# Performance work log

Measured on AMD Instinct MI355X. Metric: run time of the kernel, lower is better.

## Reference

```python
import jax, jax.numpy as jnp
import numpy as np

BN_EPS = 1e-5


def l2norm(x, axis=-1):
    # matches lavse l2norm: x / sqrt(sum(x^2)) along axis
    return x / jnp.sqrt(jnp.sum(x * x, axis=axis, keepdims=True))


def mlp(x, W1, b1, W2, b2):
    # nn.Sequential(Linear, ReLU, Linear)
    return jax.nn.relu(x @ W1 + b1) @ W2 + b2


def setup_inputs() -> dict:
    key = jax.random.key(0)
    ks = jax.random.split(key, 12)
    B, R, T, D, H = 128, 36, 64, 1024, 128  # batch, regions, max words, latent, D//k
    s = 0.02
    return {
        "img_embed": jax.random.normal(ks[0], (B, R, D), jnp.float32),
        "cap_embed": jax.random.normal(ks[1], (B, T, D), jnp.float32),
        "lens": jax.random.randint(ks[2], (B,), 1, T + 1),
        "Wg1": jax.random.normal(ks[3], (D, H), jnp.float32) * s,
        "bg1": jnp.zeros((H,), jnp.float32),
        "Wg2": jax.random.normal(ks[4], (H, D), jnp.float32) * s,
        "bg2": jnp.zeros((D,), jnp.float32),
        "Wb1": jax.random.normal(ks[5], (D, H), jnp.float32) * s,
        "bb1": jnp.zeros((H,), jnp.float32),
        "Wb2": jax.random.normal(ks[6], (H, D), jnp.float32) * s,
        "bb2": jnp.zeros((D,), jnp.float32),
    }


def reference(img_embed, cap_embed, lens, Wg1, bg1, Wg2, bg2, Wb1, bb1, Wb2, bb2):
    # img_embed: (Bi, R, D); cap_embed: (Bc, T, D); lens: (Bc,) int
    Bc, T, D = cap_embed.shape
    dt = cap_embed.dtype

    # masked mean-pool of caption words (cap_tensor[:, :n_words].mean(-1))
    mask = (jnp.arange(T)[None, :] < lens[:, None]).astype(dt)          # (Bc, T)
    cap_repr = jnp.einsum('btd,bt->bd', cap_embed, mask) / lens[:, None].astype(dt)  # (Bc, D)

    # conditional BN gamma/beta from caption representation
    gamma = mlp(cap_repr, Wg1, bg1, Wg2, bg2)                           # (Bc, D)
    beta = mlp(cap_repr, Wb1, bb1, Wb2, bb2)                            # (Bc, D)

    # BatchNorm1d(affine=False, training): per-channel stats over batch & regions
    mean = jnp.mean(img_embed, axis=(0, 1))                             # (D,)
    var = jnp.mean((img_embed - mean) ** 2, axis=(0, 1))                # biased var, (D,)
    norm_img = (img_embed - mean) / jnp.sqrt(var + BN_EPS)              # (Bi, R, D)
    norm_mean = jnp.mean(norm_img, axis=1)                              # (Bi, D), mean over regions

    # conditioned image vectors per caption: affine then l2norm
    img_vec = norm_mean[None, :, :] * (1.0 + gamma[:, None, :]) + beta[:, None, :]  # (Bc, Bi, D)
    img_vec = l2norm(img_vec, axis=-1)
    cap_vec = l2norm(cap_repr, axis=-1)                                 # (Bc, D)

    # cosine_sim(img_vector, cap_vector): dot of unit vectors; sims[:, i] = sim
    sims = jnp.einsum('cbd,cd->bc', img_vec, cap_vec)                   # (Bi, Bc)
    return sims
```

## Files before the change

### kernel.cpp

```cpp
#include <hip/hip_runtime.h>

#define DD 1024
#define TT 64
#define RR 36
#define NBC 128
#define NBI 128
#define HH 128

#define OFF_CAPR 0
#define OFF_CAPU (128 * 1024)
#define OFF_S    (2 * 128 * 1024)
#define OFF_P    (3 * 128 * 1024)
#define OFF_G1   (4 * 128 * 1024)
#define OFF_BETA (5 * 128 * 1024)
#define OFF_A    (6 * 128 * 1024)
#define OFF_BV   (6 * 128 * 1024 + 1024)
#define OFF_H    (6 * 128 * 1024 + 2048)

__device__ __forceinline__ float4 f4add(float4 a, float4 b) {
    return make_float4(a.x + b.x, a.y + b.y, a.z + b.z, a.w + b.w);
}

__global__ __launch_bounds__(256) void k_pool(const float* __restrict__ img,
                                              const float* __restrict__ cap,
                                              const int* __restrict__ lens,
                                              float* __restrict__ ws) {
    const int tid = threadIdx.x;
    const int blk = blockIdx.x;
    __shared__ float red[4];

    if (blk < NBC) {
        const int b = blk;
        const int len = lens[b];
        const float4* cp = (const float4*)(cap + (size_t)b * TT * DD);
        float4 a0 = make_float4(0.f, 0.f, 0.f, 0.f);
        float4 a1 = a0, a2 = a0, a3 = a0, a4 = a0, a5 = a0, a6 = a0, a7 = a0;
        int w = 0;
        for (; w + 8 <= len; w += 8) {
            const float4* p = cp + (size_t)w * (DD / 4) + tid;
            float4 x0 = p[0 * (DD / 4)];
            float4 x1 = p[1 * (DD / 4)];
            float4 x2 = p[2 * (DD / 4)];
            float4 x3 = p[3 * (DD / 4)];
            float4 x4 = p[4 * (DD / 4)];
            float4 x5 = p[5 * (DD / 4)];
            float4 x6 = p[6 * (DD / 4)];
            float4 x7 = p[7 * (DD / 4)];
            a0 = f4add(a0, x0); a1 = f4add(a1, x1);
            a2 = f4add(a2, x2); a3 = f4add(a3, x3);
            a4 = f4add(a4, x4); a5 = f4add(a5, x5);
            a6 = f4add(a6, x6); a7 = f4add(a7, x7);
        }
        for (; w < len; ++w) a0 = f4add(a0, cp[(size_t)w * (DD / 4) + tid]);
        float4 acc = f4add(f4add(f4add(a0, a1), f4add(a2, a3)),
                           f4add(f4add(a4, a5), f4add(a6, a7)));
        const float inv = 1.0f / (float)len;
        acc.x *= inv; acc.y *= inv; acc.z *= inv; acc.w *= inv;
        ((float4*)(ws + OFF_CAPR + (size_t)b * DD))[tid] = acc;

        float ss = acc.x * acc.x + acc.y * acc.y + acc.z * acc.z + acc.w * acc.w;
        #pragma unroll
        for (int o = 32; o; o >>= 1) ss += __shfl_xor(ss, o);
        if ((tid & 63) == 0) red[tid >> 6] = ss;
        __syncthreads();
        const float tot = red[0] + red[1] + red[2] + red[3];
        const float rn = rsqrtf(tot);
        float4 u = make_float4(acc.x * rn, acc.y * rn, acc.z * rn, acc.w * rn);
        ((float4*)(ws + OFF_CAPU + (size_t)b * DD))[tid] = u;
    } else {
        const int b = blk - NBC;
        const float4* ip = (const float4*)(img + (size_t)b * RR * DD);
        float4 s0 = make_float4(0.f, 0.f, 0.f, 0.f), s1 = s0;
        float4 q0 = s0, q1 = s0;
        #pragma unroll 3
        for (int r = 0; r < RR; r += 2) {
            float4 x = ip[r * (DD / 4) + tid];
            float4 y = ip[(r + 1) * (DD / 4) + tid];
            s0 = f4add(s0, x);
            q0.x = fmaf(x.x, x.x, q0.x); q0.y = fmaf(x.y, x.y, q0.y);
            q0.z = fmaf(x.z, x.z, q0.z); q0.w = fmaf(x.w, x.w, q0.w);
            s1 = f4add(s1, y);
            q1.x = fmaf(y.x, y.x, q1.x); q1.y = fmaf(y.y, y.y, q1.y);
            q1.z = fmaf(y.z, y.z, q1.z); q1.w = fmaf(y.w, y.w, q1.w);
        }
        ((float4*)(ws + OFF_S + (size_t)b * DD))[tid] = f4add(s0, s1);
        ((float4*)(ws + OFF_P + (size_t)b * DD))[tid] = f4add(q0, q1);
    }
}

__global__ __launch_bounds__(256) void k_mlp1(
        const float* __restrict__ Wg1, const float* __restrict__ bg1,
        const float* __restrict__ Wb1, const float* __restrict__ bb1,
        float* __restrict__ ws) {
    const int blk = blockIdx.x;
    const int tid = threadIdx.x;

    if (blk >= 256) {
        const int dl = tid & 63;
        const int d = (blk - 256) * 64 + dl;
        const int bq = tid >> 6;
        float s = 0.f, q = 0.f;
        #pragma unroll 4
        for (int i = 0; i < 32; ++i) {
            const int b = bq * 32 + i;
            s += ws[OFF_S + (size_t)b * DD + d];
            q += ws[OFF_P + (size_t)b * DD + d];
        }
        __shared__ float rs[4][64], rq[4][64];
        rs[bq][dl] = s; rq[bq][dl] = q;
        __syncthreads();
        if (bq == 0) {
            s = rs[0][dl] + rs[1][dl] + rs[2][dl] + rs[3][dl];
            q = rq[0][dl] + rq[1][dl] + rq[2][dl] + rq[3][dl];
            const float invN = 1.0f / (float)(NBI * RR);
            const float mean = s * invN;
            const float var = q * invN - mean * mean;
            const float rstd = rsqrtf(var + 1e-5f);
            ws[OFF_A + d] = rstd * (1.0f / (float)RR);
            ws[OFF_BV + d] = mean * rstd;
        }
        return;
    }

    const int cg = blk >> 4;
    const int net = (blk >> 3) & 1;
    const int jq = blk & 7;
    const int c0 = cg * 8, j0 = jq * 16;
    const int j16 = tid & 15;
    const int ks = tid >> 4;
    const float* __restrict__ W1 = net ? Wb1 : Wg1;
    const float* __restrict__ b1 = net ? bb1 : bg1;

    __shared__ float capL[8][DD];
    {
        const float4* src = (const float4*)(ws + OFF_CAPR);
        #pragma unroll
        for (int i = 0; i < 8; ++i) {
            const int idx = i * 256 + tid;
            const int c = idx >> 8, f4 = idx & 255;
            ((float4*)&capL[c][0])[f4] = src[(size_t)(c0 + c) * 256 + f4];
        }
    }
    __syncthreads();

    float a[8] = {0.f, 0.f, 0.f, 0.f, 0.f, 0.f, 0.f, 0.f};
    #pragma unroll
    for (int i = 0; i < 16; ++i) {
        const int d = i * 64 + ks * 4;
        const float w0 = W1[(size_t)(d + 0) * HH + j0 + j16];
        const float w1 = W1[(size_t)(d + 1) * HH + j0 + j16];
        const float w2 = W1[(size_t)(d + 2) * HH + j0 + j16];
        const float w3 = W1[(size_t)(d + 3) * HH + j0 + j16];
        #pragma unroll
        for (int c = 0; c < 8; ++c) {
            const float4 cv = *(const float4*)&capL[c][d];
            a[c] = fmaf(w0, cv.x, a[c]);
            a[c] = fmaf(w1, cv.y, a[c]);
            a[c] = fmaf(w2, cv.z, a[c]);
            a[c] = fmaf(w3, cv.w, a[c]);
        }
    }
    #pragma unroll
    for (int c = 0; c < 8; ++c) {
        a[c] += __shfl_xor(a[c], 16);
        a[c] += __shfl_xor(a[c], 32);
    }
    __shared__ float part[4][16][8];
    const int wv = tid >> 6;
    if ((tid & 48) == 0) {
        #pragma unroll
        for (int c = 0; c < 8; ++c) part[wv][j16][c] = a[c];
    }
    __syncthreads();
    if (tid < 128) {
        const int cc = tid >> 4, jj = tid & 15;
        float h = part[0][jj][cc] + part[1][jj][cc] + part[2][jj][cc] +
                  part[3][jj][cc] + b1[j0 + jj];
        h = fmaxf(h, 0.0f);
        ws[OFF_H + ((size_t)(c0 + cc) * 2 + net) * HH + j0 + jj] = h;
    }
}

__global__ __launch_bounds__(256) void k_mlp2(
        const float* __restrict__ Wg2, const float* __restrict__ bg2,
        const float* __restrict__ Wb2, const float* __restrict__ bb2,
        float* __restrict__ ws) {
    const int blk = blockIdx.x;
    const int cg = blk >> 4;
    const int net = (blk >> 3) & 1;
    const int dq = blk & 7;
    const int c0 = cg * 8, ch0 = dq * 128;
    const int tid = threadIdx.x;
    const float* __restrict__ W2 = net ? Wb2 : Wg2;
    const float* __restrict__ b2 = net ? bb2 : bg2;

    __shared__ float hL[8][HH];
    {
        const int c = tid >> 5, j4 = tid & 31;
        ((float4*)&hL[c][0])[j4] =
            ((const float4*)(ws + OFF_H + ((size_t)(c0 + c) * 2 + net) * HH))[j4];
    }
    __syncthreads();

    const int c = tid >> 5, q = tid & 31;
    const int ch = ch0 + q * 4;
    float4 acA = make_float4(0.f, 0.f, 0.f, 0.f);
    float4 acB = acA, acC = acA, acD = acA;
    #pragma unroll 2
    for (int j = 0; j < HH; j += 4) {
        const float4 w0 = *(const float4*)&W2[(size_t)(j + 0) * DD + ch];
        const float4 w1 = *(const float4*)&W2[(size_t)(j + 1) * DD + ch];
        const float4 w2 = *(const float4*)&W2[(size_t)(j + 2) * DD + ch];
        const float4 w3 = *(const float4*)&W2[(size_t)(j + 3) * DD + ch];
        const float h0 = hL[c][j + 0], h1 = hL[c][j + 1];
        const float h2 = hL[c][j + 2], h3 = hL[c][j + 3];
        acA.x = fmaf(h0, w0.x, acA.x); acA.y = fmaf(h0, w0.y, acA.y);
        acA.z = fmaf(h0, w0.z, acA.z); acA.w = fmaf(h0, w0.w, acA.w);
        acB.x = fmaf(h1, w1.x, acB.x); acB.y = fmaf(h1, w1.y, acB.y);
        acB.z = fmaf(h1, w1.z, acB.z); acB.w = fmaf(h1, w1.w, acB.w);
        acC.x = fmaf(h2, w2.x, acC.x); acC.y = fmaf(h2, w2.y, acC.y);
        acC.z = fmaf(h2, w2.z, acC.z); acC.w = fmaf(h2, w2.w, acC.w);
        acD.x = fmaf(h3, w3.x, acD.x); acD.y = fmaf(h3, w3.y, acD.y);
        acD.z = fmaf(h3, w3.z, acD.z); acD.w = fmaf(h3, w3.w, acD.w);
    }
    float4 acc = f4add(f4add(acA, acB), f4add(acC, acD));
    const float4 bv = *(const float4*)&b2[ch];
    if (net == 0) {
        float4 g = make_float4(1.f + acc.x + bv.x, 1.f + acc.y + bv.y,
                               1.f + acc.z + bv.z, 1.f + acc.w + bv.w);
        *(float4*)(ws + OFF_G1 + (size_t)(c0 + c) * DD + ch) = g;
    } else {
        float4 be = make_float4(acc.x + bv.x, acc.y + bv.y,
                                acc.z + bv.z, acc.w + bv.w);
        *(float4*)(ws + OFF_BETA + (size_t)(c0 + c) * DD + ch) = be;
    }
}

__global__ __launch_bounds__(256) void k_sims(const float* __restrict__ ws,
                                              float* __restrict__ out) {
    const int c = blockIdx.x;
    const int bg = blockIdx.y;
    const int lane = threadIdx.x & 63;
    const int w = threadIdx.x >> 6;

    const float4* Ap = (const float4*)(ws + OFF_A);
    const float4* Bp = (const float4*)(ws + OFF_BV);
    const float4* Gp = (const float4*)(ws + OFF_G1 + (size_t)c * DD);
    const float4* Ep = (const float4*)(ws + OFF_BETA + (size_t)c * DD);
    const float4* Up = (const float4*)(ws + OFF_CAPU + (size_t)c * DD);

    float4 AG[4], BB[4], CU[4];
    #pragma unroll
    for (int i = 0; i < 4; ++i) {
        const int idx = i * 64 + lane;
        const float4 a = Ap[idx];
        const float4 bv = Bp[idx];
        const float4 g = Gp[idx];
        const float4 be = Ep[idx];
        AG[i] = make_float4(a.x * g.x, a.y * g.y, a.z * g.z, a.w * g.w);
        BB[i] = make_float4(be.x - bv.x * g.x, be.y - bv.y * g.y,
                            be.z - bv.z * g.z, be.w - bv.w * g.w);
        CU[i] = Up[idx];
    }

    const float4* Sp = (const float4*)(ws + OFF_S);
    #pragma unroll
    for (int ib = 0; ib < 8; ++ib) {
        const int b = bg * 32 + w * 8 + ib;
        float dot = 0.f, ss = 0.f;
        #pragma unroll
        for (int i = 0; i < 4; ++i) {
            const float4 s4 = Sp[(size_t)b * (DD / 4) + i * 64 + lane];
            const float vx = fmaf(s4.x, AG[i].x, BB[i].x);
            const float vy = fmaf(s4.y, AG[i].y, BB[i].y);
            const float vz = fmaf(s4.z, AG[i].z, BB[i].z);
            const float vw = fmaf(s4.w, AG[i].w, BB[i].w);
            ss = fmaf(vx, vx, fmaf(vy, vy, fmaf(vz, vz, fmaf(vw, vw, ss))));
            dot = fmaf(vx, CU[i].x, fmaf(vy, CU[i].y,
                  fmaf(vz, CU[i].z, fmaf(vw, CU[i].w, dot))));
        }
        #pragma unroll
        for (int o = 32; o; o >>= 1) {
            dot += __shfl_xor(dot, o);
            ss += __shfl_xor(ss, o);
        }
        if (lane == 0) out[b * NBC + c] = dot * rsqrtf(ss);
    }
}

extern "C" void kernel_launch(void* const* d_in, const int* in_sizes, int n_in,
                              void* d_out, int out_size, void* d_ws, size_t ws_size,
                              hipStream_t stream) {
    const float* img = (const float*)d_in[0];
    const float* cap = (const float*)d_in[1];
    const int* lens  = (const int*)d_in[2];
    const float* Wg1 = (const float*)d_in[3];
    const float* bg1 = (const float*)d_in[4];
    const float* Wg2 = (const float*)d_in[5];
    const float* bg2 = (const float*)d_in[6];
    const float* Wb1 = (const float*)d_in[7];
    const float* bb1 = (const float*)d_in[8];
    const float* Wb2 = (const float*)d_in[9];
    const float* bb2 = (const float*)d_in[10];
    float* ws = (float*)d_ws;
    float* out = (float*)d_out;

    hipLaunchKernelGGL(k_pool, dim3(256), dim3(256), 0, stream, img, cap, lens, ws);
    hipLaunchKernelGGL(k_mlp1, dim3(272), dim3(256), 0, stream,
                       Wg1, bg1, Wb1, bb1, ws);
    hipLaunchKernelGGL(k_mlp2, dim3(256), dim3(256), 0, stream,
                       Wg2, bg2, Wb2, bb2, ws);
    hipLaunchKernelGGL(k_sims, dim3(128, 4), dim3(256), 0, stream, ws, out);
}
```

Baseline: 128.5 us.

## Fuse four kernels into one cooperative kernel with grid-wide syncs

Merges pooling, MLP layer 1, MLP layer 2 plus BN stats, and the similarity stage into one cooperative kernel of 256 blocks separated by grid.sync(). The aim is to remove three kernel launch gaps and their tail effects. MLP2 is retiled to 16 captions per block over 128 blocks, and the final stage uses 2 blocks per caption instead of 4. If the cooperative launch fails it falls back to the old four-kernel path. Grid barriers cost extra, and the heavy shared-memory footprint must still allow all 256 blocks to be co-resident.

```diff
diff --git a/kernel.cpp b/kernel.cpp
--- a/kernel.cpp
+++ b/kernel.cpp
@@ -1,4 +1,7 @@
 #include <hip/hip_runtime.h>
+#include <hip/hip_cooperative_groups.h>
+
+namespace cg = cooperative_groups;
 
 #define DD 1024
 #define TT 64
@@ -7,27 +10,38 @@
 #define NBI 128
 #define HH 128
 
+#define SEG (128 * 1024)
 #define OFF_CAPR 0
-#define OFF_CAPU (128 * 1024)
-#define OFF_S    (2 * 128 * 1024)
-#define OFF_P    (3 * 128 * 1024)
-#define OFF_G1   (4 * 128 * 1024)
-#define OFF_BETA (5 * 128 * 1024)
-#define OFF_A    (6 * 128 * 1024)
-#define OFF_BV   (6 * 128 * 1024 + 1024)
-#define OFF_H    (6 * 128 * 1024 + 2048)
+#define OFF_CAPU (1 * SEG)
+#define OFF_S    (2 * SEG)
+#define OFF_P    (3 * SEG)
+#define OFF_G1   (4 * SEG)
+#define OFF_BETA (5 * SEG)
+#define OFF_A    (6 * SEG)
+#define OFF_BV   (6 * SEG + 1024)
+#define OFF_H    (6 * SEG + 2048)
 
 __device__ __forceinline__ float4 f4add(float4 a, float4 b) {
     return make_float4(a.x + b.x, a.y + b.y, a.z + b.z, a.w + b.w);
 }
 
-__global__ __launch_bounds__(256) void k_pool(const float* __restrict__ img,
-                                              const float* __restrict__ cap,
-                                              const int* __restrict__ lens,
-                                              float* __restrict__ ws) {
+__global__ __launch_bounds__(256) void k_fused(
+        const float* __restrict__ img, const float* __restrict__ cap,
+        const int* __restrict__ lens,
+        const float* __restrict__ Wg1, const float* __restrict__ bg1,
+        const float* __restrict__ Wg2, const float* __restrict__ bg2,
+        const float* __restrict__ Wb1, const float* __restrict__ bb1,
+        const float* __restrict__ Wb2, const float* __restrict__ bb2,
+        float* __restrict__ ws, float* __restrict__ out) {
+    cg::grid_group grid = cg::this_grid();
+    const int blk = blockIdx.x;
     const int tid = threadIdx.x;
-    const int blk = blockIdx.x;
-    __shared__ float red[4];
+
+    __shared__ float capL[8][DD];
+    __shared__ float part[4][16][8];
+    __shared__ float hL[16][HH];
+    __shared__ float rs[4][64], rq[4][64];
+    __shared__ float red4[4];
 
     if (blk < NBC) {
         const int b = blk;
@@ -61,6 +75,267 @@
         float ss = acc.x * acc.x + acc.y * acc.y + acc.z * acc.z + acc.w * acc.w;
         #pragma unroll
         for (int o = 32; o; o >>= 1) ss += __shfl_xor(ss, o);
+        if ((tid & 63) == 0) red4[tid >> 6] = ss;
+        __syncthreads();
+        const float tot = red4[0] + red4[1] + red4[2] + red4[3];
+        const float rn = rsqrtf(tot);
+        float4 u = make_float4(acc.x * rn, acc.y * rn, acc.z * rn, acc.w * rn);
+        ((float4*)(ws + OFF_CAPU + (size_t)b * DD))[tid] = u;
+    } else {
+        const int b = blk - NBC;
+        const float4* ip = (const float4*)(img + (size_t)b * RR * DD);
+        float4 s0 = make_float4(0.f, 0.f, 0.f, 0.f), s1 = s0;
+        float4 q0 = s0, q1 = s0;
+        #pragma unroll 3
+        for (int r = 0; r < RR; r += 2) {
+            float4 x = ip[r * (DD / 4) + tid];
+            float4 y = ip[(r + 1) * (DD / 4) + tid];
+            s0 = f4add(s0, x);
+            q0.x = fmaf(x.x, x.x, q0.x); q0.y = fmaf(x.y, x.y, q0.y);
+            q0.z = fmaf(x.z, x.z, q0.z); q0.w = fmaf(x.w, x.w, q0.w);
+            s1 = f4add(s1, y);
+            q1.x = fmaf(y.x, y.x, q1.x); q1.y = fmaf(y.y, y.y, q1.y);
+            q1.z = fmaf(y.z, y.z, q1.z); q1.w = fmaf(y.w, y.w, q1.w);
+        }
+        ((float4*)(ws + OFF_S + (size_t)b * DD))[tid] = f4add(s0, s1);
+        ((float4*)(ws + OFF_P + (size_t)b * DD))[tid] = f4add(q0, q1);
+    }
+
+    grid.sync();
+
+    {
+        const int cg_ = blk >> 4;
+        const int net = (blk >> 3) & 1;
+        const int jq = blk & 7;
+        const int c0 = cg_ * 8, j0 = jq * 16;
+        const int j16 = tid & 15;
+        const int ks = tid >> 4;
+        const float* __restrict__ W1 = net ? Wb1 : Wg1;
+        const float* __restrict__ b1 = net ? bb1 : bg1;
+
+        {
+            const float4* src = (const float4*)(ws + OFF_CAPR);
+            #pragma unroll
+            for (int i = 0; i < 8; ++i) {
+                ((float4*)&capL[i][0])[tid] = src[(size_t)(c0 + i) * 256 + tid];
+            }
+        }
+        __syncthreads();
+
+        float a[8] = {0.f, 0.f, 0.f, 0.f, 0.f, 0.f, 0.f, 0.f};
+        #pragma unroll
+        for (int i = 0; i < 16; ++i) {
+            const int d = i * 64 + ks * 4;
+            const float w0 = W1[(size_t)(d + 0) * HH + j0 + j16];
+            const float w1 = W1[(size_t)(d + 1) * HH + j0 + j16];
+            const float w2 = W1[(size_t)(d + 2) * HH + j0 + j16];
+            const float w3 = W1[(size_t)(d + 3) * HH + j0 + j16];
+            #pragma unroll
+            for (int c = 0; c < 8; ++c) {
+                const float4 cv = *(const float4*)&capL[c][d];
+                a[c] = fmaf(w0, cv.x, a[c]);
+                a[c] = fmaf(w1, cv.y, a[c]);
+                a[c] = fmaf(w2, cv.z, a[c]);
+                a[c] = fmaf(w3, cv.w, a[c]);
+            }
+        }
+        #pragma unroll
+        for (int c = 0; c < 8; ++c) {
+            a[c] += __shfl_xor(a[c], 16);
+            a[c] += __shfl_xor(a[c], 32);
+        }
+        const int wv = tid >> 6;
+        if ((tid & 48) == 0) {
+            #pragma unroll
+            for (int c = 0; c < 8; ++c) part[wv][j16][c] = a[c];
+        }
+        __syncthreads();
+        if (tid < 128) {
+            const int cc = tid >> 4, jj = tid & 15;
+            float h = part[0][jj][cc] + part[1][jj][cc] + part[2][jj][cc] +
+                      part[3][jj][cc] + b1[j0 + jj];
+            h = fmaxf(h, 0.0f);
+            ws[OFF_H + ((size_t)(c0 + cc) * 2 + net) * HH + j0 + jj] = h;
+        }
+    }
+
+    grid.sync();
+
+    if (blk < 128) {
+        const int cg_ = blk >> 4;
+        const int net = (blk >> 3) & 1;
+        const int dq = blk & 7;
+        const int c0 = cg_ * 16, ch0 = dq * 128;
+        const float* __restrict__ W2 = net ? Wb2 : Wg2;
+        const float* __restrict__ b2 = net ? bb2 : bg2;
+
+        #pragma unroll
+        for (int i = 0; i < 2; ++i) {
+            const int idx = i * 256 + tid;
+            const int c = idx >> 5, j4 = idx & 31;
+            ((float4*)&hL[c][0])[j4] =
+                ((const float4*)(ws + OFF_H + ((size_t)(c0 + c) * 2 + net) * HH))[j4];
+        }
+        __syncthreads();
+
+        const int c = tid >> 4, q = tid & 15;
+        const int ch = ch0 + q * 8;
+        float4 a0 = make_float4(0.f, 0.f, 0.f, 0.f);
+        float4 a1 = a0, a2 = a0, a3 = a0;
+        #pragma unroll 4
+        for (int j = 0; j < HH; j += 2) {
+            const float4 w0 = *(const float4*)&W2[(size_t)j * DD + ch];
+            const float4 w1 = *(const float4*)&W2[(size_t)j * DD + ch + 4];
+            const float4 w2_ = *(const float4*)&W2[(size_t)(j + 1) * DD + ch];
+            const float4 w3 = *(const float4*)&W2[(size_t)(j + 1) * DD + ch + 4];
+            const float h0 = hL[c][j], h1 = hL[c][j + 1];
+            a0.x = fmaf(h0, w0.x, a0.x); a0.y = fmaf(h0, w0.y, a0.y);
+            a0.z = fmaf(h0, w0.z, a0.z); a0.w = fmaf(h0, w0.w, a0.w);
+            a1.x = fmaf(h0, w1.x, a1.x); a1.y = fmaf(h0, w1.y, a1.y);
+            a1.z = fmaf(h0, w1.z, a1.z); a1.w = fmaf(h0, w1.w, a1.w);
+            a2.x = fmaf(h1, w2_.x, a2.x); a2.y = fmaf(h1, w2_.y, a2.y);
+            a2.z = fmaf(h1, w2_.z, a2.z); a2.w = fmaf(h1, w2_.w, a2.w);
+            a3.x = fmaf(h1, w3.x, a3.x); a3.y = fmaf(h1, w3.y, a3.y);
+            a3.z = fmaf(h1, w3.z, a3.z); a3.w = fmaf(h1, w3.w, a3.w);
+        }
+        float4 r0 = f4add(a0, a2);
+        float4 r1 = f4add(a1, a3);
+        const float4 b2a = *(const float4*)&b2[ch];
+        const float4 b2b = *(const float4*)&b2[ch + 4];
+        if (net == 0) {
+            float4 g0 = make_float4(1.f + r0.x + b2a.x, 1.f + r0.y + b2a.y,
+                                    1.f + r0.z + b2a.z, 1.f + r0.w + b2a.w);
+            float4 g1v = make_float4(1.f + r1.x + b2b.x, 1.f + r1.y + b2b.y,
+                                     1.f + r1.z + b2b.z, 1.f + r1.w + b2b.w);
+            *(float4*)(ws + OFF_G1 + (size_t)(c0 + c) * DD + ch) = g0;
+            *(float4*)(ws + OFF_G1 + (size_t)(c0 + c) * DD + ch + 4) = g1v;
+        } else {
+            float4 e0 = make_float4(r0.x + b2a.x, r0.y + b2a.y,
+                                    r0.z + b2a.z, r0.w + b2a.w);
+            float4 e1 = make_float4(r1.x + b2b.x, r1.y + b2b.y,
+                                    r1.z + b2b.z, r1.w + b2b.w);
+            *(float4*)(ws + OFF_BETA + (size_t)(c0 + c) * DD + ch) = e0;
+            *(float4*)(ws + OFF_BETA + (size_t)(c0 + c) * DD + ch + 4) = e1;
+        }
+    } else if (blk < 144) {
+        const int dl = tid & 63;
+        const int d = (blk - 128) * 64 + dl;
+        const int bq = tid >> 6;
+        float s = 0.f, q = 0.f;
+        #pragma unroll 4
+        for (int i = 0; i < 32; ++i) {
+            const int b = bq * 32 + i;
+            s += ws[OFF_S + (size_t)b * DD + d];
+            q += ws[OFF_P + (size_t)b * DD + d];
+        }
+        rs[bq][dl] = s; rq[bq][dl] = q;
+        __syncthreads();
+        if (bq == 0) {
+            s = rs[0][dl] + rs[1][dl] + rs[2][dl] + rs[3][dl];
+            q = rq[0][dl] + rq[1][dl] + rq[2][dl] + rq[3][dl];
+            const float invN = 1.0f / (float)(NBI * RR);
+            const float mean = s * invN;
+            const float var = q * invN - mean * mean;
+            const float rstd = rsqrtf(var + 1e-5f);
+            ws[OFF_A + d] = rstd * (1.0f / (float)RR);
+            ws[OFF_BV + d] = mean * rstd;
+        }
+    }
+
+    grid.sync();
+
+    {
+        const int c = blk >> 1;
+        const int bg = blk & 1;
+        const int lane = tid & 63;
+        const int w = tid >> 6;
+
+        const float4* Ap = (const float4*)(ws + OFF_A);
+        const float4* Bp = (const float4*)(ws + OFF_BV);
+        const float4* Gp = (const float4*)(ws + OFF_G1 + (size_t)c * DD);
+        const float4* Ep = (const float4*)(ws + OFF_BETA + (size_t)c * DD);
+        const float4* Up = (const float4*)(ws + OFF_CAPU + (size_t)c * DD);
+
+        float4 AG[4], BB[4], CU[4];
+        #pragma unroll
+        for (int i = 0; i < 4; ++i) {
+            const int idx = i * 64 + lane;
+            const float4 a = Ap[idx];
+            const float4 bv = Bp[idx];
+            const float4 g = Gp[idx];
+            const float4 be = Ep[idx];
+            AG[i] = make_float4(a.x * g.x, a.y * g.y, a.z * g.z, a.w * g.w);
+            BB[i] = make_float4(be.x - bv.x * g.x, be.y - bv.y * g.y,
+                                be.z - bv.z * g.z, be.w - bv.w * g.w);
+            CU[i] = Up[idx];
+        }
+
+        const float4* Sp = (const float4*)(ws + OFF_S);
+        #pragma unroll
+        for (int ib = 0; ib < 16; ++ib) {
+            const int b = bg * 64 + w * 16 + ib;
+            float dot = 0.f, ss = 0.f;
+            #pragma unroll
+            for (int i = 0; i < 4; ++i) {
+                const float4 s4 = Sp[(size_t)b * (DD / 4) + i * 64 + lane];
+                const float vx = fmaf(s4.x, AG[i].x, BB[i].x);
+                const float vy = fmaf(s4.y, AG[i].y, BB[i].y);
+                const float vz = fmaf(s4.z, AG[i].z, BB[i].z);
+                const float vw = fmaf(s4.w, AG[i].w, BB[i].w);
+                ss = fmaf(vx, vx, fmaf(vy, vy, fmaf(vz, vz, fmaf(vw, vw, ss))));
+                dot = fmaf(vx, CU[i].x, fmaf(vy, CU[i].y,
+                      fmaf(vz, CU[i].z, fmaf(vw, CU[i].w, dot))));
+            }
+            #pragma unroll
+            for (int o = 32; o; o >>= 1) {
+                dot += __shfl_xor(dot, o);
+                ss += __shfl_xor(ss, o);
+            }
+            if (lane == 0) out[b * NBC + c] = dot * rsqrtf(ss);
+        }
+    }
+}
+
+__global__ __launch_bounds__(256) void k_pool(const float* __restrict__ img,
+                                              const float* __restrict__ cap,
+                                              const int* __restrict__ lens,
+                                              float* __restrict__ ws) {
+    const int tid = threadIdx.x;
+    const int blk = blockIdx.x;
+    __shared__ float red[4];
+
+    if (blk < NBC) {
+        const int b = blk;
+        const int len = lens[b];
+        const float4* cp = (const float4*)(cap + (size_t)b * TT * DD);
+        float4 a0 = make_float4(0.f, 0.f, 0.f, 0.f);
+        float4 a1 = a0, a2 = a0, a3 = a0, a4 = a0, a5 = a0, a6 = a0, a7 = a0;
+        int w = 0;
+        for (; w + 8 <= len; w += 8) {
+            const float4* p = cp + (size_t)w * (DD / 4) + tid;
+            float4 x0 = p[0 * (DD / 4)];
+            float4 x1 = p[1 * (DD / 4)];
+            float4 x2 = p[2 * (DD / 4)];
+            float4 x3 = p[3 * (DD / 4)];
+            float4 x4 = p[4 * (DD / 4)];
+            float4 x5 = p[5 * (DD / 4)];
+            float4 x6 = p[6 * (DD / 4)];
+            float4 x7 = p[7 * (DD / 4)];
+            a0 = f4add(a0, x0); a1 = f4add(a1, x1);
+            a2 = f4add(a2, x2); a3 = f4add(a3, x3);
+            a4 = f4add(a4, x4); a5 = f4add(a5, x5);
+            a6 = f4add(a6, x6); a7 = f4add(a7, x7);
+        }
+        for (; w < len; ++w) a0 = f4add(a0, cp[(size_t)w * (DD / 4) + tid]);
+        float4 acc = f4add(f4add(f4add(a0, a1), f4add(a2, a3)),
+                           f4add(f4add(a4, a5), f4add(a6, a7)));
+        const float inv = 1.0f / (float)len;
+        acc.x *= inv; acc.y *= inv; acc.z *= inv; acc.w *= inv;
+        ((float4*)(ws + OFF_CAPR + (size_t)b * DD))[tid] = acc;
+
+        float ss = acc.x * acc.x + acc.y * acc.y + acc.z * acc.z + acc.w * acc.w;
+        #pragma unroll
+        for (int o = 32; o; o >>= 1) ss += __shfl_xor(ss, o);
         if ((tid & 63) == 0) red[tid >> 6] = ss;
         __syncthreads();
         const float tot = red[0] + red[1] + red[2] + red[3];
@@ -122,10 +397,10 @@
         return;
     }
 
-    const int cg = blk >> 4;
+    const int cg_ = blk >> 4;
     const int net = (blk >> 3) & 1;
     const int jq = blk & 7;
-    const int c0 = cg * 8, j0 = jq * 16;
+    const int c0 = cg_ * 8, j0 = jq * 16;
     const int j16 = tid & 15;
     const int ks = tid >> 4;
     const float* __restrict__ W1 = net ? Wb1 : Wg1;
@@ -136,9 +411,7 @@
         const float4* src = (const float4*)(ws + OFF_CAPR);
         #pragma unroll
         for (int i = 0; i < 8; ++i) {
-            const int idx = i * 256 + tid;
-            const int c = idx >> 8, f4 = idx & 255;
-            ((float4*)&capL[c][0])[f4] = src[(size_t)(c0 + c) * 256 + f4];
+            ((float4*)&capL[i][0])[tid] = src[(size_t)(c0 + i) * 256 + tid];
         }
     }
     __syncthreads();
@@ -186,10 +459,10 @@
         const float* __restrict__ Wb2, const float* __restrict__ bb2,
         float* __restrict__ ws) {
     const int blk = blockIdx.x;
-    const int cg = blk >> 4;
+    const int cg_ = blk >> 4;
     const int net = (blk >> 3) & 1;
     const int dq = blk & 7;
-    const int c0 = cg * 8, ch0 = dq * 128;
+    const int c0 = cg_ * 8, ch0 = dq * 128;
     const int tid = threadIdx.x;
     const float* __restrict__ W2 = net ? Wb2 : Wg2;
     const float* __restrict__ b2 = net ? bb2 : bg2;
@@ -305,10 +578,21 @@
     float* ws = (float*)d_ws;
     float* out = (float*)d_out;
 
-    hipLaunchKernelGGL(k_pool, dim3(256), dim3(256), 0, stream, img, cap, lens, ws);
-    hipLaunchKernelGGL(k_mlp1, dim3(272), dim3(256), 0, stream,
-                       Wg1, bg1, Wb1, bb1, ws);
-    hipLaunchKernelGGL(k_mlp2, dim3(256), dim3(256), 0, stream,
-                       Wg2, bg2, Wb2, bb2, ws);
-    hipLaunchKernelGGL(k_sims, dim3(128, 4), dim3(256), 0, stream, ws, out);
-}
+    void* args[] = {(void*)&img, (void*)&cap, (void*)&lens,
+                    (void*)&Wg1, (void*)&bg1, (void*)&Wg2, (void*)&bg2,
+                    (void*)&Wb1, (void*)&bb1, (void*)&Wb2, (void*)&bb2,
+                    (void*)&ws, (void*)&out};
+    hipError_t err = hipLaunchCooperativeKernel((const void*)k_fused,
+                                                dim3(256), dim3(256),
+                                                args, 0, stream);
+    if (err != hipSuccess) {
+        (void)hipGetLastError();
+        hipLaunchKernelGGL(k_pool, dim3(256), dim3(256), 0, stream,
+                           img, cap, lens, ws);
+        hipLaunchKernelGGL(k_mlp1, dim3(272), dim3(256), 0, stream,
+                           Wg1, bg1, Wb1, bb1, ws);
+        hipLaunchKernelGGL(k_mlp2, dim3(256), dim3(256), 0, stream,
+                           Wg2, bg2, Wb2, bb2, ws);
+        hipLaunchKernelGGL(k_sims, dim3(128, 4), dim3(256), 0, stream, ws, out);
+    }
+}
```

After: 241.6 us. +88.1%, slower.

## Split pooling into halves and fuse MLP second layer with similarity kernel

Applied to the files above, without the earlier changes.

The pooling kernel now splits each caption and image batch element across two blocks, writing partial sums that later stages combine. This doubles parallelism in the bandwidth-bound first stage. The second MLP layer is fused into the similarity kernel, so each caption block computes gamma/beta in registers and shared memory, removing one launch and the gamma/beta round trip through global memory. The trade-off is that the final kernel has only 128 blocks, and each block streams both full W2 matrices and all 128 image rows, which may limit parallelism.

```diff
diff --git a/kernel.cpp b/kernel.cpp
--- a/kernel.cpp
+++ b/kernel.cpp
@@ -7,18 +7,24 @@
 #define NBI 128
 #define HH 128
 
-#define OFF_CAPR 0
-#define OFF_CAPU (128 * 1024)
-#define OFF_S    (2 * 128 * 1024)
-#define OFF_P    (3 * 128 * 1024)
-#define OFF_G1   (4 * 128 * 1024)
-#define OFF_BETA (5 * 128 * 1024)
-#define OFF_A    (6 * 128 * 1024)
-#define OFF_BV   (6 * 128 * 1024 + 1024)
-#define OFF_H    (6 * 128 * 1024 + 2048)
+#define SEG (128 * 1024)
+#define OFF_CP0 (0 * SEG)
+#define OFF_CP1 (1 * SEG)
+#define OFF_S0  (2 * SEG)
+#define OFF_S1  (3 * SEG)
+#define OFF_P0  (4 * SEG)
+#define OFF_P1  (5 * SEG)
+#define OFF_S   (6 * SEG)
+#define OFF_A   (7 * SEG)
+#define OFF_BV  (7 * SEG + 1024)
+#define OFF_H   (7 * SEG + 2048)
 
 __device__ __forceinline__ float4 f4add(float4 a, float4 b) {
     return make_float4(a.x + b.x, a.y + b.y, a.z + b.z, a.w + b.w);
+}
+__device__ __forceinline__ float4 f4fma(float s, float4 w, float4 a) {
+    return make_float4(fmaf(s, w.x, a.x), fmaf(s, w.y, a.y),
+                       fmaf(s, w.z, a.z), fmaf(s, w.w, a.w));
 }
 
 __global__ __launch_bounds__(256) void k_pool(const float* __restrict__ img,
@@ -27,16 +33,17 @@
                                               float* __restrict__ ws) {
     const int tid = threadIdx.x;
     const int blk = blockIdx.x;
-    __shared__ float red[4];
-
-    if (blk < NBC) {
-        const int b = blk;
+
+    if (blk < 256) {
+        const int b = blk >> 1, h = blk & 1;
         const int len = lens[b];
+        const int w0 = h * 32;
+        const int w1 = min(len, w0 + 32);
         const float4* cp = (const float4*)(cap + (size_t)b * TT * DD);
         float4 a0 = make_float4(0.f, 0.f, 0.f, 0.f);
         float4 a1 = a0, a2 = a0, a3 = a0, a4 = a0, a5 = a0, a6 = a0, a7 = a0;
-        int w = 0;
-        for (; w + 8 <= len; w += 8) {
+        int w = w0;
+        for (; w + 8 <= w1; w += 8) {
             const float4* p = cp + (size_t)w * (DD / 4) + tid;
             float4 x0 = p[0 * (DD / 4)];
             float4 x1 = p[1 * (DD / 4)];
@@ -51,29 +58,20 @@
             a4 = f4add(a4, x4); a5 = f4add(a5, x5);
             a6 = f4add(a6, x6); a7 = f4add(a7, x7);
         }
-        for (; w < len; ++w) a0 = f4add(a0, cp[(size_t)w * (DD / 4) + tid]);
+        for (; w < w1; ++w) a0 = f4add(a0, cp[(size_t)w * (DD / 4) + tid]);
         float4 acc = f4add(f4add(f4add(a0, a1), f4add(a2, a3)),
                            f4add(f4add(a4, a5), f4add(a6, a7)));
-        const float inv = 1.0f / (float)len;
-        acc.x *= inv; acc.y *= inv; acc.z *= inv; acc.w *= inv;
-        ((float4*)(ws + OFF_CAPR + (size_t)b * DD))[tid] = acc;
-
-        float ss = acc.x * acc.x + acc.y * acc.y + acc.z * acc.z + acc.w * acc.w;
-        #pragma unroll
-        for (int o = 32; o; o >>= 1) ss += __shfl_xor(ss, o);
-        if ((tid & 63) == 0) red[tid >> 6] = ss;
-        __syncthreads();
-        const float tot = red[0] + red[1] + red[2] + red[3];
-        const float rn = rsqrtf(tot);
-        float4 u = make_float4(acc.x * rn, acc.y * rn, acc.z * rn, acc.w * rn);
-        ((float4*)(ws + OFF_CAPU + (size_t)b * DD))[tid] = u;
+        float* dst = ws + (h ? OFF_CP1 : OFF_CP0) + (size_t)b * DD;
+        ((float4*)dst)[tid] = acc;
     } else {
-        const int b = blk - NBC;
-        const float4* ip = (const float4*)(img + (size_t)b * RR * DD);
+        const int t = blk - 256;
+        const int b = t >> 1, h = t & 1;
+        const float4* ip = (const float4*)(img + (size_t)b * RR * DD +
+                                           (size_t)h * 18 * DD);
         float4 s0 = make_float4(0.f, 0.f, 0.f, 0.f), s1 = s0;
         float4 q0 = s0, q1 = s0;
         #pragma unroll 3
-        for (int r = 0; r < RR; r += 2) {
+        for (int r = 0; r < 18; r += 2) {
             float4 x = ip[r * (DD / 4) + tid];
             float4 y = ip[(r + 1) * (DD / 4) + tid];
             s0 = f4add(s0, x);
@@ -83,17 +81,32 @@
             q1.x = fmaf(y.x, y.x, q1.x); q1.y = fmaf(y.y, y.y, q1.y);
             q1.z = fmaf(y.z, y.z, q1.z); q1.w = fmaf(y.w, y.w, q1.w);
         }
-        ((float4*)(ws + OFF_S + (size_t)b * DD))[tid] = f4add(s0, s1);
-        ((float4*)(ws + OFF_P + (size_t)b * DD))[tid] = f4add(q0, q1);
-    }
-}
-
-__global__ __launch_bounds__(256) void k_mlp1(
+        float* sd = ws + (h ? OFF_S1 : OFF_S0) + (size_t)b * DD;
+        float* pd = ws + (h ? OFF_P1 : OFF_P0) + (size_t)b * DD;
+        ((float4*)sd)[tid] = f4add(s0, s1);
+        ((float4*)pd)[tid] = f4add(q0, q1);
+    }
+}
+
+__global__ __launch_bounds__(256) void k_mid(
         const float* __restrict__ Wg1, const float* __restrict__ bg1,
         const float* __restrict__ Wb1, const float* __restrict__ bb1,
+        const int* __restrict__ lens,
         float* __restrict__ ws) {
     const int blk = blockIdx.x;
     const int tid = threadIdx.x;
+
+    __shared__ float capL[8][DD];
+    __shared__ float part[4][16][8];
+    __shared__ float rs[4][64], rq[4][64];
+
+    if (blk >= 272) {
+        const int b = blk - 272;
+        float4 s0 = ((const float4*)(ws + OFF_S0 + (size_t)b * DD))[tid];
+        float4 s1 = ((const float4*)(ws + OFF_S1 + (size_t)b * DD))[tid];
+        ((float4*)(ws + OFF_S + (size_t)b * DD))[tid] = f4add(s0, s1);
+        return;
+    }
 
     if (blk >= 256) {
         const int dl = tid & 63;
@@ -103,10 +116,9 @@
         #pragma unroll 4
         for (int i = 0; i < 32; ++i) {
             const int b = bq * 32 + i;
-            s += ws[OFF_S + (size_t)b * DD + d];
-            q += ws[OFF_P + (size_t)b * DD + d];
-        }
-        __shared__ float rs[4][64], rq[4][64];
+            s += ws[OFF_S0 + (size_t)b * DD + d] + ws[OFF_S1 + (size_t)b * DD + d];
+            q += ws[OFF_P0 + (size_t)b * DD + d] + ws[OFF_P1 + (size_t)b * DD + d];
+        }
         rs[bq][dl] = s; rq[bq][dl] = q;
         __syncthreads();
         if (bq == 0) {
@@ -122,24 +134,24 @@
         return;
     }
 
-    const int cg = blk >> 4;
+    const int cg_ = blk >> 4;
     const int net = (blk >> 3) & 1;
     const int jq = blk & 7;
-    const int c0 = cg * 8, j0 = jq * 16;
+    const int c0 = cg_ * 8, j0 = jq * 16;
     const int j16 = tid & 15;
     const int ks = tid >> 4;
     const float* __restrict__ W1 = net ? Wb1 : Wg1;
     const float* __restrict__ b1 = net ? bb1 : bg1;
 
-    __shared__ float capL[8][DD];
-    {
-        const float4* src = (const float4*)(ws + OFF_CAPR);
-        #pragma unroll
-        for (int i = 0; i < 8; ++i) {
-            const int idx = i * 256 + tid;
-            const int c = idx >> 8, f4 = idx & 255;
-            ((float4*)&capL[c][0])[f4] = src[(size_t)(c0 + c) * 256 + f4];
-        }
+    #pragma unroll
+    for (int i = 0; i < 8; ++i) {
+        const int cc = c0 + i;
+        const float invl = 1.0f / (float)lens[cc];
+        float4 p0 = ((const float4*)(ws + OFF_CP0 + (size_t)cc * DD))[tid];
+        float4 p1 = ((const float4*)(ws + OFF_CP1 + (size_t)cc * DD))[tid];
+        ((float4*)&capL[i][0])[tid] =
+            make_float4((p0.x + p1.x) * invl, (p0.y + p1.y) * invl,
+                        (p0.z + p1.z) * invl, (p0.w + p1.w) * invl);
     }
     __syncthreads();
 
@@ -165,7 +177,6 @@
         a[c] += __shfl_xor(a[c], 16);
         a[c] += __shfl_xor(a[c], 32);
     }
-    __shared__ float part[4][16][8];
     const int wv = tid >> 6;
     if ((tid & 48) == 0) {
         #pragma unroll
@@ -181,93 +192,81 @@
     }
 }
 
-__global__ __launch_bounds__(256) void k_mlp2(
+__global__ __launch_bounds__(256) void k_out(
         const float* __restrict__ Wg2, const float* __restrict__ bg2,
         const float* __restrict__ Wb2, const float* __restrict__ bb2,
-        float* __restrict__ ws) {
-    const int blk = blockIdx.x;
-    const int cg = blk >> 4;
-    const int net = (blk >> 3) & 1;
-    const int dq = blk & 7;
-    const int c0 = cg * 8, ch0 = dq * 128;
+        const int* __restrict__ lens,
+        const float* __restrict__ ws, float* __restrict__ out) {
+    const int c = blockIdx.x;
     const int tid = threadIdx.x;
-    const float* __restrict__ W2 = net ? Wb2 : Wg2;
-    const float* __restrict__ b2 = net ? bb2 : bg2;
-
-    __shared__ float hL[8][HH];
-    {
-        const int c = tid >> 5, j4 = tid & 31;
-        ((float4*)&hL[c][0])[j4] =
-            ((const float4*)(ws + OFF_H + ((size_t)(c0 + c) * 2 + net) * HH))[j4];
-    }
+    const int lane = tid & 63;
+    const int w = tid >> 6;
+
+    __shared__ float hgL[HH], hbL[HH];
+    __shared__ float4 CUl[256];
+    __shared__ float4 AGl[256];
+    __shared__ float4 BBl[256];
+    __shared__ float red4[4];
+
+    if (tid < 128) hgL[tid] = ws[OFF_H + ((size_t)c * 2 + 0) * HH + tid];
+    else hbL[tid - 128] = ws[OFF_H + ((size_t)c * 2 + 1) * HH + (tid - 128)];
+
+    const float invl = 1.0f / (float)lens[c];
+    float4 p0 = ((const float4*)(ws + OFF_CP0 + (size_t)c * DD))[tid];
+    float4 p1 = ((const float4*)(ws + OFF_CP1 + (size_t)c * DD))[tid];
+    float4 cr = make_float4((p0.x + p1.x) * invl, (p0.y + p1.y) * invl,
+                            (p0.z + p1.z) * invl, (p0.w + p1.w) * invl);
+    float ss = cr.x * cr.x + cr.y * cr.y + cr.z * cr.z + cr.w * cr.w;
+    #pragma unroll
+    for (int o = 32; o; o >>= 1) ss += __shfl_xor(ss, o);
+    if (lane == 0) red4[w] = ss;
     __syncthreads();
-
-    const int c = tid >> 5, q = tid & 31;
-    const int ch = ch0 + q * 4;
-    float4 acA = make_float4(0.f, 0.f, 0.f, 0.f);
-    float4 acB = acA, acC = acA, acD = acA;
+    const float rn = rsqrtf(red4[0] + red4[1] + red4[2] + red4[3]);
+    CUl[tid] = make_float4(cr.x * rn, cr.y * rn, cr.z * rn, cr.w * rn);
+
+    const float4* W2gf = (const float4*)Wg2;
+    const float4* W2bf = (const float4*)Wb2;
+    float4 ag0 = make_float4(0.f, 0.f, 0.f, 0.f);
+    float4 ag1 = ag0, ab0 = ag0, ab1 = ag0;
     #pragma unroll 2
-    for (int j = 0; j < HH; j += 4) {
-        const float4 w0 = *(const float4*)&W2[(size_t)(j + 0) * DD + ch];
-        const float4 w1 = *(const float4*)&W2[(size_t)(j + 1) * DD + ch];
-        const float4 w2 = *(const float4*)&W2[(size_t)(j + 2) * DD + ch];
-        const float4 w3 = *(const float4*)&W2[(size_t)(j + 3) * DD + ch];
-        const float h0 = hL[c][j + 0], h1 = hL[c][j + 1];
-        const float h2 = hL[c][j + 2], h3 = hL[c][j + 3];
-        acA.x = fmaf(h0, w0.x, acA.x); acA.y = fmaf(h0, w0.y, acA.y);
-        acA.z = fmaf(h0, w0.z, acA.z); acA.w = fmaf(h0, w0.w, acA.w);
-        acB.x = fmaf(h1, w1.x, acB.x); acB.y = fmaf(h1, w1.y, acB.y);
-        acB.z = fmaf(h1, w1.z, acB.z); acB.w = fmaf(h1, w1.w, acB.w);
-        acC.x = fmaf(h2, w2.x, acC.x); acC.y = fmaf(h2, w2.y, acC.y);
-        acC.z = fmaf(h2, w2.z, acC.z); acC.w = fmaf(h2, w2.w, acC.w);
-        acD.x = fmaf(h3, w3.x, acD.x); acD.y = fmaf(h3, w3.y, acD.y);
-        acD.z = fmaf(h3, w3.z, acD.z); acD.w = fmaf(h3, w3.w, acD.w);
-    }
-    float4 acc = f4add(f4add(acA, acB), f4add(acC, acD));
-    const float4 bv = *(const float4*)&b2[ch];
-    if (net == 0) {
-        float4 g = make_float4(1.f + acc.x + bv.x, 1.f + acc.y + bv.y,
-                               1.f + acc.z + bv.z, 1.f + acc.w + bv.w);
-        *(float4*)(ws + OFF_G1 + (size_t)(c0 + c) * DD + ch) = g;
-    } else {
-        float4 be = make_float4(acc.x + bv.x, acc.y + bv.y,
-                                acc.z + bv.z, acc.w + bv.w);
-        *(float4*)(ws + OFF_BETA + (size_t)(c0 + c) * DD + ch) = be;
-    }
-}
-
-__global__ __launch_bounds__(256) void k_sims(const float* __restrict__ ws,
-                                              float* __restrict__ out) {
-    const int c = blockIdx.x;
-    const int bg = blockIdx.y;
-    const int lane = threadIdx.x & 63;
-    const int w = threadIdx.x >> 6;
-
-    const float4* Ap = (const float4*)(ws + OFF_A);
-    const float4* Bp = (const float4*)(ws + OFF_BV);
-    const float4* Gp = (const float4*)(ws + OFF_G1 + (size_t)c * DD);
-    const float4* Ep = (const float4*)(ws + OFF_BETA + (size_t)c * DD);
-    const float4* Up = (const float4*)(ws + OFF_CAPU + (size_t)c * DD);
+    for (int j = 0; j < HH; j += 2) {
+        const float hg0 = hgL[j], hg1 = hgL[j + 1];
+        const float hb0 = hbL[j], hb1 = hbL[j + 1];
+        const float4 wg0 = W2gf[(size_t)j * 256 + tid];
+        const float4 wg1 = W2gf[(size_t)(j + 1) * 256 + tid];
+        const float4 wb0 = W2bf[(size_t)j * 256 + tid];
+        const float4 wb1 = W2bf[(size_t)(j + 1) * 256 + tid];
+        ag0 = f4fma(hg0, wg0, ag0); ag1 = f4fma(hg1, wg1, ag1);
+        ab0 = f4fma(hb0, wb0, ab0); ab1 = f4fma(hb1, wb1, ab1);
+    }
+    const float4 ga = f4add(ag0, ag1);
+    const float4 ba = f4add(ab0, ab1);
+    const float4 bgv = ((const float4*)bg2)[tid];
+    const float4 bbv = ((const float4*)bb2)[tid];
+    const float4 g1 = make_float4(1.f + ga.x + bgv.x, 1.f + ga.y + bgv.y,
+                                  1.f + ga.z + bgv.z, 1.f + ga.w + bgv.w);
+    const float4 be = make_float4(ba.x + bbv.x, ba.y + bbv.y,
+                                  ba.z + bbv.z, ba.w + bbv.w);
+    const float4 A4 = ((const float4*)(ws + OFF_A))[tid];
+    const float4 BV4 = ((const float4*)(ws + OFF_BV))[tid];
+    AGl[tid] = make_float4(A4.x * g1.x, A4.y * g1.y, A4.z * g1.z, A4.w * g1.w);
+    BBl[tid] = make_float4(be.x - BV4.x * g1.x, be.y - BV4.y * g1.y,
+                           be.z - BV4.z * g1.z, be.w - BV4.w * g1.w);
+    __syncthreads();
 
     float4 AG[4], BB[4], CU[4];
     #pragma unroll
     for (int i = 0; i < 4; ++i) {
-        const int idx = i * 64 + lane;
-        const float4 a = Ap[idx];
-        const float4 bv = Bp[idx];
-        const float4 g = Gp[idx];
-        const float4 be = Ep[idx];
-        AG[i] = make_float4(a.x * g.x, a.y * g.y, a.z * g.z, a.w * g.w);
-        BB[i] = make_float4(be.x - bv.x * g.x, be.y - bv.y * g.y,
-                            be.z - bv.z * g.z, be.w - bv.w * g.w);
-        CU[i] = Up[idx];
+        AG[i] = AGl[i * 64 + lane];
+        BB[i] = BBl[i * 64 + lane];
+        CU[i] = CUl[i * 64 + lane];
     }
 
     const float4* Sp = (const float4*)(ws + OFF_S);
-    #pragma unroll
-    for (int ib = 0; ib < 8; ++ib) {
-        const int b = bg * 32 + w * 8 + ib;
-        float dot = 0.f, ss = 0.f;
+    #pragma unroll 4
+    for (int ib = 0; ib < 32; ++ib) {
+        const int b = w * 32 + ib;
+        float dot = 0.f, s2 = 0.f;
         #pragma unroll
         for (int i = 0; i < 4; ++i) {
             const float4 s4 = Sp[(size_t)b * (DD / 4) + i * 64 + lane];
@@ -275,16 +274,16 @@
             const float vy = fmaf(s4.y, AG[i].y, BB[i].y);
             const float vz = fmaf(s4.z, AG[i].z, BB[i].z);
             const float vw = fmaf(s4.w, AG[i].w, BB[i].w);
-            ss = fmaf(vx, vx, fmaf(vy, vy, fmaf(vz, vz, fmaf(vw, vw, ss))));
+            s2 = fmaf(vx, vx, fmaf(vy, vy, fmaf(vz, vz, fmaf(vw, vw, s2))));
             dot = fmaf(vx, CU[i].x, fmaf(vy, CU[i].y,
                   fmaf(vz, CU[i].z, fmaf(vw, CU[i].w, dot))));
         }
         #pragma unroll
         for (int o = 32; o; o >>= 1) {
             dot += __shfl_xor(dot, o);
-            ss += __shfl_xor(ss, o);
-        }
-        if (lane == 0) out[b * NBC + c] = dot * rsqrtf(ss);
+            s2 += __shfl_xor(s2, o);
+        }
+        if (lane == 0) out[b * NBC + c] = dot * rsqrtf(s2);
     }
 }
 
@@ -305,10 +304,10 @@
     float* ws = (float*)d_ws;
     float* out = (float*)d_out;
 
-    hipLaunchKernelGGL(k_pool, dim3(256), dim3(256), 0, stream, img, cap, lens, ws);
-    hipLaunchKernelGGL(k_mlp1, dim3(272), dim3(256), 0, stream,
-                       Wg1, bg1, Wb1, bb1, ws);
-    hipLaunchKernelGGL(k_mlp2, dim3(256), dim3(256), 0, stream,
-                       Wg2, bg2, Wb2, bb2, ws);
-    hipLaunchKernelGGL(k_sims, dim3(128, 4), dim3(256), 0, stream, ws, out);
-}
+    hipLaunchKernelGGL(k_pool, dim3(512), dim3(256), 0, stream,
+                       img, cap, lens, ws);
+    hipLaunchKernelGGL(k_mid, dim3(400), dim3(256), 0, stream,
+                       Wg1, bg1, Wb1, bb1, lens, ws);
+    hipLaunchKernelGGL(k_out, dim3(128), dim3(256), 0, stream,
+                       Wg2, bg2, Wb2, bb2, lens, ws, out);
+}
```

New measurement: 145.1 us. 1.13x slower.
